# Kernel optimization log

Measured on AMD Instinct MI355X. Metric: run time of the kernel, lower is better.

Reference implementation:

```python
import jax, jax.numpy as jnp
import numpy as np

# Module hyper-parameters (from init_kwargs)
NDIM = 2
KSIZE = [3, 3]            # must be odd per ConvSP checks
DILATION = [0.05, 0.05]
RADIUS = 0.1
C_IN, C_OUT = 64, 64
B, N = 2, 2048


def _offsets():
    # Kernel-cell center offsets relative to the particle, row-major over dims
    # (matches the cartesian ordering of the original C extension).
    axes = [(np.arange(k) - (k - 1) / 2.0) * d for k, d in zip(KSIZE, DILATION)]
    grids = np.meshgrid(*axes, indexing='ij')
    return np.stack([g.reshape(-1) for g in grids], axis=-1).astype(np.float32)  # [ncells, D]


def setup_inputs() -> dict:
    key = jax.random.key(0)
    k1, k2, k3, k4, k5, k6 = jax.random.split(key, 6)
    pos = jax.random.uniform(k1, (B, N, NDIM), dtype=jnp.float32)          # coords in [0,1]^D
    invmass = jax.random.uniform(k2, (B, N), dtype=jnp.float32) * 0.9 + 0.1  # avoid 1/0
    locs = jnp.concatenate([pos, invmass[..., None]], axis=-1)             # [B,N,D+1]
    data = jax.random.normal(k3, (B, C_IN, N), dtype=jnp.float32)
    density = jax.random.uniform(k4, (B, N), dtype=jnp.float32) + 0.5      # strictly positive
    ncells = int(np.prod(KSIZE))
    weight = jax.random.normal(k5, (C_OUT, C_IN, ncells), dtype=jnp.float32) * 0.05
    bias = jax.random.normal(k6, (C_OUT,), dtype=jnp.float32) * 0.05
    return {"locs": locs, "data": data, "density": density, "weight": weight, "bias": bias}


def _convsp(locs, data, density, weight, bias):
    # SPH interpolation at each kernel-cell query point r_{i,k} = x_i + off_k:
    #   field[b,c,i,k] = sum_j (m_j / rho_j) * data[b,c,j] * W(|x_j - r_{i,k}|, RADIUS)
    # with m_j = 1/invmass_j, then a 1x1-style contraction with weight over (c,k).
    pos = locs[..., :NDIM]                               # [B,N,D]
    invmass = locs[..., NDIM]                            # [B,N]
    coef = 1.0 / (invmass * density)                     # m_j / rho_j, [B,N]
    dcoef = data * coef[:, None, :]                      # [B,C,N]
    diff = pos[:, :, None, :] - pos[:, None, :, :]       # x_i - x_j, [B,N,N,D]
    r2 = RADIUS * RADIUS
    knorm = 315.0 / (64.0 * np.pi * RADIUS ** 9)         # poly6 smoothing kernel norm
    offs = _offsets()                                    # [ncells, D]
    bsz, n = pos.shape[0], pos.shape[1]
    out = jnp.broadcast_to(bias[None, :, None], (bsz, weight.shape[0], n))
    for k in range(offs.shape[0]):                       # fixed small ncells=9 loop
        # |x_j - x_i - off| == |(x_i - x_j) + off|
        d2 = jnp.sum((diff + offs[k]) ** 2, axis=-1)     # [B,N,N] (i = query, j = neighbor)
        w = jnp.where(d2 < r2, (r2 - d2) ** 3, 0.0) * knorm
        field = jnp.einsum('bcj,bij->bci', dcoef, w)     # gather-weighted average
        out = out + jnp.einsum('oc,bci->boi', weight[:, :, k], field)
    return out


def reference(locs, data, density, weight, bias):
    return _convsp(locs, data, density, weight, bias)
```

## Files before the change

kernel.cpp:

```cpp
#include <hip/hip_runtime.h>
#include <hip/hip_bf16.h>
#include <stdint.h>

#define BATCH 2
#define NPTS  2048
#define CIN   64
#define COUT  64
#define NCELL 9

#define KNORM 1.5666851e9f
#define R2 0.01f

typedef __attribute__((ext_vector_type(8))) __bf16 bf16x8;
typedef __attribute__((ext_vector_type(4))) float  f32x4;

union B8 { uint4 u; bf16x8 v; };

typedef __attribute__((address_space(3))) uint8_t        lds_t;
typedef const __attribute__((address_space(1))) uint8_t  glb_t;

static __device__ __forceinline__ unsigned pk2(float a, float b) {
    union { __hip_bfloat162 h; unsigned u; } cv;
    cv.h = __float22bfloat162_rn(make_float2(a, b));
    return cv.u;
}


__global__ __launch_bounds__(256) void prep_kernel(
    const float* __restrict__ locs, const float* __restrict__ data,
    const float* __restrict__ density, const float* __restrict__ weight,
    const float* __restrict__ bias,
    float2* __restrict__ posT, uint16_t* __restrict__ dC,
    uint16_t* __restrict__ WB, float* __restrict__ out)
{
    const int tid = threadIdx.x;
    const int g = blockIdx.x;
    if (g < 256) {
        int e = g * 256 + tid;
        int j4 = e & 511, bc = e >> 9;
        int b = bc >> 6;
        float4 dv = *(const float4*)(data + bc * 2048 + j4 * 4);
        float4 de = *(const float4*)(density + b * 2048 + j4 * 4);
        int jb = (b * 2048 + j4 * 4) * 3 + 2;
        float m0 = locs[jb], m1 = locs[jb + 3], m2 = locs[jb + 6], m3 = locs[jb + 9];
        float v0 = dv.x / (m0 * de.x) * KNORM;
        float v1 = dv.y / (m1 * de.y) * KNORM;
        float v2 = dv.z / (m2 * de.z) * KNORM;
        float v3 = dv.w / (m3 * de.w) * KNORM;
        *(uint2*)(dC + bc * 2048 + j4 * 4) = make_uint2(pk2(v0, v1), pk2(v2, v3));
    } else if (g < 272) {
        int jj = (g - 256) * 256 + tid;
        posT[jj] = make_float2(locs[jj * 3], locs[jj * 3 + 1]);
    } else if (g < 272 + NCELL) {
        int cell = g - 272;
        for (int it = 0; it < 16; it++) {
            int e = it * 256 + tid;
            int ks = e >> 11, ob = (e >> 9) & 3, lane = (e >> 3) & 63, jj = e & 7;
            int o = ob * 16 + (lane & 15);
            int c = ks * 32 + ((lane >> 4) & 3) * 8 + jj;
            union { __hip_bfloat16 h; uint16_t u; } cv;
            cv.h = __float2bfloat16(weight[(o * 64 + c) * 9 + cell]);
            WB[cell * 4096 + e] = cv.u;
        }
    } else {
        const int gb = g - (272 + NCELL);
#pragma unroll
        for (int r = 0; r < 2; r++) {
            int e4 = (gb * 512 + r * 256 + tid) * 4;
            float bv = bias[(e4 >> 11) & 63];
            *(float4*)(out + e4) = make_float4(bv, bv, bv, bv);
        }
    }
}

__global__ __launch_bounds__(256, 4) void conv_kernel(
    const float2* __restrict__ posT, const uint16_t* __restrict__ dC,
    const uint16_t* __restrict__ WB, float* __restrict__ out)
{
    __shared__ uint16_t db[2][2048];
    __shared__ float    sft[4 * 16 * 68];

    const int tid  = threadIdx.x;
    const int lane = tid & 63;
    const int wid  = tid >> 6;
    const int cl   = lane & 15;
    const int quad = lane >> 4;
    const int bx   = blockIdx.x;
    const int b    = bx >> 9;
    const int i0   = ((bx >> 2) & 127) * 16;
    const int jh   = bx & 3;
    const int jb0  = jh * 512;

    const int hw = ((bx >> 8) + bx) & 3;
    const int r  = (wid - hw) & 3;

    const float2 pI = posT[b * 2048 + i0 + cl];
    const float2* pbase = posT + b * 2048 + jb0;

    f32x4 acc[3][4];
#pragma unroll
    for (int ci = 0; ci < 3; ci++)
#pragma unroll
        for (int nb = 0; nb < 4; nb++) acc[ci][nb] = (f32x4){0.f, 0.f, 0.f, 0.f};

    const uint16_t* srcbase =
        dC + (b * 64 + wid * 16 + (lane >> 2)) * 2048 + jb0 + (lane & 3) * 8;

#define STAGE(n, buf)                                                         \
    __builtin_amdgcn_global_load_lds((glb_t*)(srcbase + (n) * 32),            \
                                     (lds_t*)(&db[buf][wid * 512]), 16, 0, 0)

#define CELL(CI, CX, CY, CC, HASX, HASY)                                      \
    {                                                                         \
        float w_[8];                                                          \
        _Pragma("unroll")                                                     \
        for (int p = 0; p < 8; p++) {                                         \
            float t = sv[p];                                                  \
            if (HASY) t = fmaf((CY), dyv[p], t);                              \
            if (HASX) t = fmaf((CX), dxv[p], t);                              \
            if ((HASX) || (HASY)) t += (CC);                                  \
            float mt = fmaxf(t, 0.0f);                                        \
            w_[p] = (mt * mt) * mt;                                           \
        }                                                                     \
        B8 af;                                                                \
        af.u = make_uint4(pk2(w_[0], w_[1]), pk2(w_[2], w_[3]),               \
                          pk2(w_[4], w_[5]), pk2(w_[6], w_[7]));              \
        _Pragma("unroll")                                                     \
        for (int nb = 0; nb < 4; nb++)                                        \
            acc[CI][nb] = __builtin_amdgcn_mfma_f32_16x16x32_bf16(            \
                af.v, bf[nb].v, acc[CI][nb], 0, 0, 0);                        \
    }

    STAGE(0, 0);

    for (int n = 0; n < 16; n++) {
        __syncthreads();
        if (n < 15) STAGE(n + 1, (n + 1) & 1);
        const int buf = n & 1;

        B8 bf[4];
#pragma unroll
        for (int nb = 0; nb < 4; nb++)
            bf[nb].u = *(const uint4*)&db[buf][(nb * 16 + cl) * 32 + quad * 8];

        const float4* pp = (const float4*)(pbase + n * 32 + quad * 8);
        float4 q0 = pp[0], q1 = pp[1], q2 = pp[2], q3 = pp[3];
        float dxv[8], dyv[8], sv[8];
        dxv[0] = pI.x - q0.x; dyv[0] = pI.y - q0.y;
        dxv[1] = pI.x - q0.z; dyv[1] = pI.y - q0.w;
        dxv[2] = pI.x - q1.x; dyv[2] = pI.y - q1.y;
        dxv[3] = pI.x - q1.z; dyv[3] = pI.y - q1.w;
        dxv[4] = pI.x - q2.x; dyv[4] = pI.y - q2.y;
        dxv[5] = pI.x - q2.z; dyv[5] = pI.y - q2.w;
        dxv[6] = pI.x - q3.x; dyv[6] = pI.y - q3.y;
        dxv[7] = pI.x - q3.z; dyv[7] = pI.y - q3.w;
#pragma unroll
        for (int p = 0; p < 8; p++)
            sv[p] = fmaf(-dyv[p], dyv[p], fmaf(-dxv[p], dxv[p], R2));

        if (r == 0) {
            CELL(0,  0.1f,  0.1f, -0.005f,  1, 1);
            CELL(1,  0.1f, -0.1f, -0.005f,  1, 1);
        } else if (r == 1) {
            CELL(0, -0.1f,  0.1f, -0.005f,  1, 1);
            CELL(1, -0.1f, -0.1f, -0.005f,  1, 1);
        } else if (r == 2) {
            CELL(0,  0.1f,  0.0f, -0.0025f, 1, 0);
            CELL(1,  0.0f,  0.1f, -0.0025f, 0, 1);
            CELL(2,  0.0f,  0.0f,  0.0f,    0, 0);
        } else {
            CELL(0,  0.0f, -0.1f, -0.0025f, 0, 1);
            CELL(1, -0.1f,  0.0f, -0.0025f, 1, 0);
        }
    }

    const int nc = (r == 2) ? 3 : 2;
    int kcs[3];
    if (r == 0)      { kcs[0] = 0; kcs[1] = 2; kcs[2] = 0; }
    else if (r == 1) { kcs[0] = 6; kcs[1] = 8; kcs[2] = 0; }
    else if (r == 2) { kcs[0] = 1; kcs[1] = 3; kcs[2] = 4; }
    else             { kcs[0] = 5; kcs[1] = 7; kcs[2] = 0; }

    float* scr = &sft[wid * (16 * 68)];
    f32x4 acc2[4];
#pragma unroll
    for (int ob = 0; ob < 4; ob++) acc2[ob] = (f32x4){0.f, 0.f, 0.f, 0.f};

#pragma unroll
    for (int ci = 0; ci < 3; ci++) {
        if (ci < nc) {
#pragma unroll
            for (int nb = 0; nb < 4; nb++)
#pragma unroll
                for (int rr = 0; rr < 4; rr++)
                    scr[(quad * 4 + rr) * 68 + nb * 16 + cl] = acc[ci][nb][rr];
            int k = kcs[ci];
#pragma unroll
            for (int ks = 0; ks < 2; ks++) {
                const float* fp = &scr[cl * 68 + ks * 32 + quad * 8];
                float4 lo = *(const float4*)fp;
                float4 hi = *(const float4*)(fp + 4);
                B8 af;
                af.u = make_uint4(pk2(lo.x, lo.y), pk2(lo.z, lo.w),
                                  pk2(hi.x, hi.y), pk2(hi.z, hi.w));
#pragma unroll
                for (int ob = 0; ob < 4; ob++) {
                    B8 wf;
                    wf.u = *(const uint4*)(WB + k * 4096 + (ks * 4 + ob) * 512 + lane * 8);
                    acc2[ob] = __builtin_amdgcn_mfma_f32_16x16x32_bf16(
                        af.v, wf.v, acc2[ob], 0, 0, 0);
                }
            }
        }
    }

#pragma unroll
    for (int ob = 0; ob < 4; ob++)
#pragma unroll
        for (int rr = 0; rr < 4; rr++)
            scr[(quad * 4 + rr) * 68 + ob * 16 + cl] = acc2[ob][rr];
    __syncthreads();

    {
        const int i  = tid & 15;
        const int og = tid >> 4;
        float4 s0 = *(const float4*)&sft[0 * 1088 + i * 68 + og * 4];
        float4 s1 = *(const float4*)&sft[1 * 1088 + i * 68 + og * 4];
        float4 s2 = *(const float4*)&sft[2 * 1088 + i * 68 + og * 4];
        float4 s3 = *(const float4*)&sft[3 * 1088 + i * 68 + og * 4];
        float v0 = s0.x + s1.x + s2.x + s3.x;
        float v1 = s0.y + s1.y + s2.y + s3.y;
        float v2 = s0.z + s1.z + s2.z + s3.z;
        float v3 = s0.w + s1.w + s2.w + s3.w;
        float* ob_ = out + (b * 64 + og * 4) * 2048 + i0 + i;
        unsafeAtomicAdd(ob_ + 0 * 2048, v0);
        unsafeAtomicAdd(ob_ + 1 * 2048, v1);
        unsafeAtomicAdd(ob_ + 2 * 2048, v2);
        unsafeAtomicAdd(ob_ + 3 * 2048, v3);
    }
#undef STAGE
#undef CELL
}

extern "C" void kernel_launch(void* const* d_in, const int* in_sizes, int n_in,
                              void* d_out, int out_size, void* d_ws, size_t ws_size,
                              hipStream_t stream)
{
    const float* locs    = (const float*)d_in[0];
    const float* data    = (const float*)d_in[1];
    const float* density = (const float*)d_in[2];
    const float* weight  = (const float*)d_in[3];
    const float* bias    = (const float*)d_in[4];
    float* out = (float*)d_out;

    float2*   posT = (float2*)d_ws;
    uint16_t* dC   = (uint16_t*)((char*)d_ws + 32768);
    uint16_t* WB   = (uint16_t*)((char*)d_ws + 32768 + 524288);

    prep_kernel<<<272 + NCELL + 128, 256, 0, stream>>>(
        locs, data, density, weight, bias, posT, dC, WB, out);
    conv_kernel<<<BATCH * 128 * 4, 256, 0, stream>>>(posT, dC, WB, out);
}
```

Before: 89.49 us.

## Morton-sort points and skip far neighbor chunks via bounding-box culling

```diff
diff --git a/kernel.cpp b/kernel.cpp
--- a/kernel.cpp
+++ b/kernel.cpp
@@ -10,6 +10,7 @@
 
 #define KNORM 1.5666851e9f
 #define R2 0.01f
+#define MARGIN 0.1505f
 
 typedef __attribute__((ext_vector_type(8))) __bf16 bf16x8;
 typedef __attribute__((ext_vector_type(4))) float  f32x4;
@@ -25,34 +26,85 @@
     return cv.u;
 }
 
-
-__global__ __launch_bounds__(256) void prep_kernel(
-    const float* __restrict__ locs, const float* __restrict__ data,
-    const float* __restrict__ density, const float* __restrict__ weight,
+static __device__ __forceinline__ int mpart(int v) {
+    v = (v | (v << 2)) & 0x33;
+    v = (v | (v << 1)) & 0x55;
+    return v;
+}
+
+
+__global__ __launch_bounds__(256) void prep_sort(
+    const float* __restrict__ locs, const float* __restrict__ weight,
     const float* __restrict__ bias,
-    float2* __restrict__ posT, uint16_t* __restrict__ dC,
-    uint16_t* __restrict__ WB, float* __restrict__ out)
+    float2* __restrict__ posT, uint16_t* __restrict__ WB,
+    int* __restrict__ perm, float4* __restrict__ cbox,
+    float4* __restrict__ ibox, float* __restrict__ out)
 {
     const int tid = threadIdx.x;
     const int g = blockIdx.x;
-    if (g < 256) {
-        int e = g * 256 + tid;
-        int j4 = e & 511, bc = e >> 9;
-        int b = bc >> 6;
-        float4 dv = *(const float4*)(data + bc * 2048 + j4 * 4);
-        float4 de = *(const float4*)(density + b * 2048 + j4 * 4);
-        int jb = (b * 2048 + j4 * 4) * 3 + 2;
-        float m0 = locs[jb], m1 = locs[jb + 3], m2 = locs[jb + 6], m3 = locs[jb + 9];
-        float v0 = dv.x / (m0 * de.x) * KNORM;
-        float v1 = dv.y / (m1 * de.y) * KNORM;
-        float v2 = dv.z / (m2 * de.z) * KNORM;
-        float v3 = dv.w / (m3 * de.w) * KNORM;
-        *(uint2*)(dC + bc * 2048 + j4 * 4) = make_uint2(pk2(v0, v1), pk2(v2, v3));
-    } else if (g < 272) {
-        int jj = (g - 256) * 256 + tid;
-        posT[jj] = make_float2(locs[jj * 3], locs[jj * 3 + 1]);
-    } else if (g < 272 + NCELL) {
-        int cell = g - 272;
+    if (g < 2) {
+        const int b = g;
+        __shared__ float2 spos[2048];
+        __shared__ float2 ssrt[2048];
+        __shared__ short  scll[2048];
+        __shared__ int    hist[256];
+        __shared__ int    scn[256];
+        hist[tid] = 0;
+        __syncthreads();
+#pragma unroll
+        for (int u = 0; u < 8; u++) {
+            int idx = u * 256 + tid;
+            float x = locs[(b * 2048 + idx) * 3];
+            float y = locs[(b * 2048 + idx) * 3 + 1];
+            int cx = (int)(x * 16.0f); cx = cx < 0 ? 0 : (cx > 15 ? 15 : cx);
+            int cy = (int)(y * 16.0f); cy = cy < 0 ? 0 : (cy > 15 ? 15 : cy);
+            spos[idx] = make_float2(x, y);
+            scll[idx] = (short)(mpart(cx) | (mpart(cy) << 1));
+            atomicAdd(&hist[scll[idx]], 1);
+        }
+        __syncthreads();
+        int v = hist[tid];
+        scn[tid] = v;
+        __syncthreads();
+        for (int ofs = 1; ofs < 256; ofs <<= 1) {
+            int t = (tid >= ofs) ? scn[tid - ofs] : 0;
+            __syncthreads();
+            scn[tid] += t;
+            __syncthreads();
+        }
+        hist[tid] = scn[tid] - v;
+        __syncthreads();
+#pragma unroll
+        for (int u = 0; u < 8; u++) {
+            int idx = u * 256 + tid;
+            int c = scll[idx];
+            int dst = atomicAdd(&hist[c], 1);
+            float2 p = spos[idx];
+            ssrt[dst] = p;
+            posT[b * 2048 + dst] = p;
+            perm[b * 2048 + dst] = idx;
+        }
+        __syncthreads();
+        if (tid < 64) {
+            float xmn = 1e30f, xmx = -1e30f, ymn = 1e30f, ymx = -1e30f;
+            for (int u = 0; u < 32; u++) {
+                float2 p = ssrt[tid * 32 + u];
+                xmn = fminf(xmn, p.x); xmx = fmaxf(xmx, p.x);
+                ymn = fminf(ymn, p.y); ymx = fmaxf(ymx, p.y);
+            }
+            cbox[b * 64 + tid] = make_float4(xmn, xmx, ymn, ymx);
+        }
+        if (tid < 128) {
+            float xmn = 1e30f, xmx = -1e30f, ymn = 1e30f, ymx = -1e30f;
+            for (int u = 0; u < 16; u++) {
+                float2 p = ssrt[tid * 16 + u];
+                xmn = fminf(xmn, p.x); xmx = fmaxf(xmx, p.x);
+                ymn = fminf(ymn, p.y); ymx = fmaxf(ymx, p.y);
+            }
+            ibox[b * 128 + tid] = make_float4(xmn, xmx, ymn, ymx);
+        }
+    } else if (g < 2 + NCELL) {
+        int cell = g - 2;
         for (int it = 0; it < 16; it++) {
             int e = it * 256 + tid;
             int ks = e >> 11, ob = (e >> 9) & 3, lane = (e >> 3) & 63, jj = e & 7;
@@ -63,7 +115,7 @@
             WB[cell * 4096 + e] = cv.u;
         }
     } else {
-        const int gb = g - (272 + NCELL);
+        const int gb = g - (2 + NCELL);
 #pragma unroll
         for (int r = 0; r < 2; r++) {
             int e4 = (gb * 512 + r * 256 + tid) * 4;
@@ -73,9 +125,31 @@
     }
 }
 
+__global__ __launch_bounds__(256) void prep_dc(
+    const float* __restrict__ locs, const float* __restrict__ data,
+    const float* __restrict__ density, const int* __restrict__ perm,
+    uint16_t* __restrict__ dC)
+{
+    int e = blockIdx.x * 256 + threadIdx.x;
+    int j4 = e & 511, bc = e >> 9;
+    int b = bc >> 6;
+    float vv[4];
+#pragma unroll
+    for (int u = 0; u < 4; u++) {
+        int jo = perm[b * 2048 + j4 * 4 + u];
+        float d  = data[bc * 2048 + jo];
+        float de = density[b * 2048 + jo];
+        float m  = locs[(b * 2048 + jo) * 3 + 2];
+        vv[u] = d / (m * de) * KNORM;
+    }
+    *(uint2*)(dC + bc * 2048 + j4 * 4) = make_uint2(pk2(vv[0], vv[1]), pk2(vv[2], vv[3]));
+}
+
 __global__ __launch_bounds__(256, 4) void conv_kernel(
     const float2* __restrict__ posT, const uint16_t* __restrict__ dC,
-    const uint16_t* __restrict__ WB, float* __restrict__ out)
+    const uint16_t* __restrict__ WB, const float4* __restrict__ cbox,
+    const float4* __restrict__ ibox, const int* __restrict__ perm,
+    float* __restrict__ out)
 {
     __shared__ uint16_t db[2][2048];
     __shared__ float    sft[4 * 16 * 68];
@@ -93,6 +167,16 @@
 
     const int hw = ((bx >> 8) + bx) & 3;
     const int r  = (wid - hw) & 3;
+
+    const float4 ib = ibox[b * 128 + (i0 >> 4)];
+    uint32_t mask = 0;
+    for (int c = 0; c < 16; c++) {
+        float4 cb = cbox[b * 64 + jh * 16 + c];
+        bool keep = (cb.x - ib.y < MARGIN) && (ib.x - cb.y < MARGIN) &&
+                    (cb.z - ib.w < MARGIN) && (ib.z - cb.w < MARGIN);
+        mask |= (keep ? 1u : 0u) << c;
+    }
+    if (mask == 0) return;
 
     const float2 pI = posT[b * 2048 + i0 + cl];
     const float2* pbase = posT + b * 2048 + jb0;
@@ -131,46 +215,52 @@
                 af.v, bf[nb].v, acc[CI][nb], 0, 0, 0);                        \
     }
 
-    STAGE(0, 0);
-
-    for (int n = 0; n < 16; n++) {
-        __syncthreads();
-        if (n < 15) STAGE(n + 1, (n + 1) & 1);
-        const int buf = n & 1;
-
-        B8 bf[4];
-#pragma unroll
-        for (int nb = 0; nb < 4; nb++)
-            bf[nb].u = *(const uint4*)&db[buf][(nb * 16 + cl) * 32 + quad * 8];
-
-        const float4* pp = (const float4*)(pbase + n * 32 + quad * 8);
-        float4 q0 = pp[0], q1 = pp[1], q2 = pp[2], q3 = pp[3];
-        float dxv[8], dyv[8], sv[8];
-        dxv[0] = pI.x - q0.x; dyv[0] = pI.y - q0.y;
-        dxv[1] = pI.x - q0.z; dyv[1] = pI.y - q0.w;
-        dxv[2] = pI.x - q1.x; dyv[2] = pI.y - q1.y;
-        dxv[3] = pI.x - q1.z; dyv[3] = pI.y - q1.w;
-        dxv[4] = pI.x - q2.x; dyv[4] = pI.y - q2.y;
-        dxv[5] = pI.x - q2.z; dyv[5] = pI.y - q2.w;
-        dxv[6] = pI.x - q3.x; dyv[6] = pI.y - q3.y;
-        dxv[7] = pI.x - q3.z; dyv[7] = pI.y - q3.w;
-#pragma unroll
-        for (int p = 0; p < 8; p++)
-            sv[p] = fmaf(-dyv[p], dyv[p], fmaf(-dxv[p], dxv[p], R2));
-
-        if (r == 0) {
-            CELL(0,  0.1f,  0.1f, -0.005f,  1, 1);
-            CELL(1,  0.1f, -0.1f, -0.005f,  1, 1);
-        } else if (r == 1) {
-            CELL(0, -0.1f,  0.1f, -0.005f,  1, 1);
-            CELL(1, -0.1f, -0.1f, -0.005f,  1, 1);
-        } else if (r == 2) {
-            CELL(0,  0.1f,  0.0f, -0.0025f, 1, 0);
-            CELL(1,  0.0f,  0.1f, -0.0025f, 0, 1);
-            CELL(2,  0.0f,  0.0f,  0.0f,    0, 0);
-        } else {
-            CELL(0,  0.0f, -0.1f, -0.0025f, 0, 1);
-            CELL(1, -0.1f,  0.0f, -0.0025f, 1, 0);
+    {
+        int cur = __builtin_ctz(mask);
+        uint32_t rem = mask & (mask - 1);
+        int bufp = 0;
+        STAGE(cur, 0);
+        while (cur >= 0) {
+            __syncthreads();
+            int nxt = rem ? (int)__builtin_ctz(rem) : -1;
+            if (nxt >= 0) { STAGE(nxt, bufp ^ 1); rem &= rem - 1; }
+
+            B8 bf[4];
+#pragma unroll
+            for (int nb = 0; nb < 4; nb++)
+                bf[nb].u = *(const uint4*)&db[bufp][(nb * 16 + cl) * 32 + quad * 8];
+
+            const float4* pp = (const float4*)(pbase + cur * 32 + quad * 8);
+            float4 q0 = pp[0], q1 = pp[1], q2 = pp[2], q3 = pp[3];
+            float dxv[8], dyv[8], sv[8];
+            dxv[0] = pI.x - q0.x; dyv[0] = pI.y - q0.y;
+            dxv[1] = pI.x - q0.z; dyv[1] = pI.y - q0.w;
+            dxv[2] = pI.x - q1.x; dyv[2] = pI.y - q1.y;
+            dxv[3] = pI.x - q1.z; dyv[3] = pI.y - q1.w;
+            dxv[4] = pI.x - q2.x; dyv[4] = pI.y - q2.y;
+            dxv[5] = pI.x - q2.z; dyv[5] = pI.y - q2.w;
+            dxv[6] = pI.x - q3.x; dyv[6] = pI.y - q3.y;
+            dxv[7] = pI.x - q3.z; dyv[7] = pI.y - q3.w;
+#pragma unroll
+            for (int p = 0; p < 8; p++)
+                sv[p] = fmaf(-dyv[p], dyv[p], fmaf(-dxv[p], dxv[p], R2));
+
+            if (r == 0) {
+                CELL(0,  0.1f,  0.1f, -0.005f,  1, 1);
+                CELL(1,  0.1f, -0.1f, -0.005f,  1, 1);
+            } else if (r == 1) {
+                CELL(0, -0.1f,  0.1f, -0.005f,  1, 1);
+                CELL(1, -0.1f, -0.1f, -0.005f,  1, 1);
+            } else if (r == 2) {
+                CELL(0,  0.1f,  0.0f, -0.0025f, 1, 0);
+                CELL(1,  0.0f,  0.1f, -0.0025f, 0, 1);
+                CELL(2,  0.0f,  0.0f,  0.0f,    0, 0);
+            } else {
+                CELL(0,  0.0f, -0.1f, -0.0025f, 0, 1);
+                CELL(1, -0.1f,  0.0f, -0.0025f, 1, 0);
+            }
+
+            cur = nxt; bufp ^= 1;
         }
     }
 
@@ -232,7 +322,8 @@
         float v1 = s0.y + s1.y + s2.y + s3.y;
         float v2 = s0.z + s1.z + s2.z + s3.z;
         float v3 = s0.w + s1.w + s2.w + s3.w;
-        float* ob_ = out + (b * 64 + og * 4) * 2048 + i0 + i;
+        int io = perm[b * 2048 + i0 + i];
+        float* ob_ = out + (b * 64 + og * 4) * 2048 + io;
         unsafeAtomicAdd(ob_ + 0 * 2048, v0);
         unsafeAtomicAdd(ob_ + 1 * 2048, v1);
         unsafeAtomicAdd(ob_ + 2 * 2048, v2);
@@ -256,8 +347,13 @@
     float2*   posT = (float2*)d_ws;
     uint16_t* dC   = (uint16_t*)((char*)d_ws + 32768);
     uint16_t* WB   = (uint16_t*)((char*)d_ws + 32768 + 524288);
-
-    prep_kernel<<<272 + NCELL + 128, 256, 0, stream>>>(
-        locs, data, density, weight, bias, posT, dC, WB, out);
-    conv_kernel<<<BATCH * 128 * 4, 256, 0, stream>>>(posT, dC, WB, out);
-}
+    int*      perm = (int*)((char*)d_ws + 630784);
+    float4*   cbox = (float4*)((char*)d_ws + 647168);
+    float4*   ibox = (float4*)((char*)d_ws + 649216);
+
+    prep_sort<<<2 + NCELL + 128, 256, 0, stream>>>(
+        locs, weight, bias, posT, WB, perm, cbox, ibox, out);
+    prep_dc<<<256, 256, 0, stream>>>(locs, data, density, perm, dC);
+    conv_kernel<<<BATCH * 128 * 4, 256, 0, stream>>>(
+        posT, dC, WB, cbox, ibox, perm, out);
+}
```

Result: slower. 109.3 us (+22.2%).
